# Performance work log

Hardware: AMD Instinct MI355X
Metric: run time of the kernel (lower is better)

Reference implementation:

```python
import jax, jax.numpy as jnp
import numpy as np

N_NODES = 50000
N_EDGES = 1_600_000
D_IN = 128
D_OUT = 128


def setup_inputs() -> dict:
    key = jax.random.key(0)
    k1, k2, k3, k4 = jax.random.split(key, 4)
    x = jax.random.normal(k1, (N_NODES, D_IN), dtype=jnp.float32)
    weight = jax.random.normal(k2, (D_IN, D_OUT), dtype=jnp.float32)
    bias = jnp.zeros((D_OUT,), dtype=jnp.float32)
    edge_row = jax.random.randint(k3, (N_EDGES,), 0, N_NODES, dtype=jnp.int64 if jax.config.jax_enable_x64 else jnp.int32)
    edge_col = jax.random.randint(k4, (N_EDGES,), 0, N_NODES, dtype=jnp.int64 if jax.config.jax_enable_x64 else jnp.int32)
    return {"x": x, "weight": weight, "bias": bias, "edge_row": edge_row, "edge_col": edge_col}


def reference(x, weight, bias, edge_row, edge_col):
    # edges_sparse is a binary [N, N] COO adjacency; edge (row=i, col=j) has value 1.
    n = x.shape[0]
    ones = jnp.ones(edge_row.shape[0], dtype=x.dtype)
    # out_degree = A.sum(dim=1): row sums of the adjacency
    out_degree = jax.ops.segment_sum(ones, edge_row, num_segments=n)
    deg_inv_sqrt = out_degree ** -0.5  # D = diag(deg^-0.5)
    # (D A D) x  ==  scatter_i sum_j deg_i^-0.5 * deg_j^-0.5 * x_j over edges (i, j)
    w = deg_inv_sqrt[edge_row] * deg_inv_sqrt[edge_col]  # [E]
    msg = w[:, None] * x[edge_col]                        # [E, D_IN]
    agg = jax.ops.segment_sum(msg, edge_row, num_segments=n)  # [N, D_IN]
    # dense projection + bias
    return agg @ weight + bias
```

## Files before the change

kernel.cpp:

```cpp
#include <hip/hip_runtime.h>
#include <hip/hip_bf16.h>

#define NODES   50000
#define EDGES   1600000
#define DIM     128
#define NB      391
#define BSTRIDE 4608
#define TILE    4096
#define EPT     16
#define NTILES  391
#define ZROW    50000

typedef unsigned int   u32;
typedef unsigned short u16;
typedef __attribute__((ext_vector_type(4))) float f32x4;
typedef __attribute__((ext_vector_type(8))) short s16x8;

__device__ inline u16 f2bf(float f) {
  __hip_bfloat16 h = __float2bfloat16(f);
  return *reinterpret_cast<u16*>(&h);
}

__global__ __launch_bounds__(256) void k_prep(const float* __restrict__ W,
                                              u16* __restrict__ wts,
                                              int* __restrict__ gcursor) {
  __shared__ float T[32 * 132];
  int t = threadIdx.x;
  int gi = blockIdx.x * 256 + t;
  if (gi < NB) gcursor[gi] = 0;
  int c0 = blockIdx.x * 32;
#pragma unroll
  for (int i = 0; i < 16; ++i) {
    int idx = i * 256 + t;
    int k = idx >> 5;
    int cc = idx & 31;
    T[cc * 132 + k] = W[k * 128 + c0 + cc];
  }
  __syncthreads();
#pragma unroll
  for (int i = 0; i < 2; ++i) {
    int idx = i * 256 + t;
    int cc = idx >> 4;
    int kc = idx & 15;
    int c = c0 + cc;
    int kbase = kc * 8;
    u32 p[4];
#pragma unroll
    for (int u = 0; u < 4; ++u) {
      float a = T[cc * 132 + kbase + 2 * u];
      float b = T[cc * 132 + kbase + 2 * u + 1];
      p[u] = (u32)f2bf(a) | ((u32)f2bf(b) << 16);
    }
    int off = c * 256 + ((kbase * 2) ^ ((c & 15) << 4));
    *(uint4*)((char*)wts + off) = make_uint4(p[0], p[1], p[2], p[3]);
  }
}

__global__ __launch_bounds__(256) void k_binA(const int* __restrict__ erow,
                                              const int* __restrict__ ecol,
                                              int* __restrict__ gcursor,
                                              u32* __restrict__ binned) {
  __shared__ int hist[NB];
  __shared__ int lcur[NB];
  int t = threadIdx.x;
  for (int b = t; b < NB; b += 256) hist[b] = 0;
  __syncthreads();
  int base = blockIdx.x * TILE;
  u32 v[EPT];
#pragma unroll
  for (int k = 0; k < 4; ++k) {
    int e4 = base + k * 1024 + t * 4;
    if (e4 < EDGES) {
      int4 rr = *(const int4*)&erow[e4];
      int4 cc = *(const int4*)&ecol[e4];
      v[k * 4 + 0] = ((u32)rr.x << 16) | (u32)cc.x;
      v[k * 4 + 1] = ((u32)rr.y << 16) | (u32)cc.y;
      v[k * 4 + 2] = ((u32)rr.z << 16) | (u32)cc.z;
      v[k * 4 + 3] = ((u32)rr.w << 16) | (u32)cc.w;
      atomicAdd(&hist[(u32)rr.x >> 7], 1);
      atomicAdd(&hist[(u32)rr.y >> 7], 1);
      atomicAdd(&hist[(u32)rr.z >> 7], 1);
      atomicAdd(&hist[(u32)rr.w >> 7], 1);
    } else {
      v[k * 4 + 0] = 0xffffffffu;
      v[k * 4 + 1] = 0xffffffffu;
      v[k * 4 + 2] = 0xffffffffu;
      v[k * 4 + 3] = 0xffffffffu;
    }
  }
  __syncthreads();
  for (int b = t; b < NB; b += 256) {
    int h = hist[b];
    lcur[b] = h ? (b * BSTRIDE + atomicAdd(&gcursor[b], h)) : 0;
  }
  __syncthreads();
#pragma unroll
  for (int k = 0; k < EPT; ++k) {
    if (v[k] != 0xffffffffu) {
      int b = (int)(v[k] >> 23);
      int pos = atomicAdd(&lcur[b], 1);
      if (pos < (b + 1) * BSTRIDE) binned[pos] = v[k];
    }
  }
}

__global__ __launch_bounds__(512) void k_binB(const u32* __restrict__ binned,
                                              const int* __restrict__ gcur,
                                              int2* __restrict__ rp2,
                                              float* __restrict__ dis,
                                              u16* __restrict__ cols) {
  __shared__ int cnt[128];
  __shared__ int sc[128];
  __shared__ int lcur[128];
  __shared__ u16 stage[BSTRIDE];
  int b = blockIdx.x;
  int t = threadIdx.x;
  int n0 = b << 7;
  int s = b * BSTRIDE;
  int cntE = gcur[b];
  if (cntE > BSTRIDE) cntE = BSTRIDE;
  int e = s + cntE;
  if (t < 128) cnt[t] = 0;
  __syncthreads();
  u32 held[9];
#pragma unroll
  for (int k = 0; k < 9; ++k) {
    int j = s + t + k * 512;
    u32 v = (j < e) ? binned[j] : 0xffffffffu;
    held[k] = v;
    if (v != 0xffffffffu) atomicAdd(&cnt[(int)(v >> 16) - n0], 1);
  }
  __syncthreads();
  if (t < 128) sc[t] = cnt[t];
  __syncthreads();
  for (int off = 1; off < 128; off <<= 1) {
    int tmp = (t >= off && t < 128) ? sc[t - off] : 0;
    __syncthreads();
    if (t < 128) sc[t] += tmp;
    __syncthreads();
  }
  if (t < 128) {
    int n = n0 + t;
    if (n < NODES) {
      int lexcl = sc[t] - cnt[t];
      rp2[n] = make_int2(s + lexcl, s + lexcl + cnt[t]);
      lcur[t] = lexcl;
      dis[n] = rsqrtf((float)cnt[t]);
    }
  }
  __syncthreads();
#pragma unroll
  for (int k = 0; k < 9; ++k) {
    u32 v = held[k];
    if (v != 0xffffffffu) {
      int pos = atomicAdd(&lcur[(int)(v >> 16) - n0], 1);
      stage[pos] = (u16)(v & 0xffffu);
    }
  }
  __syncthreads();
  {
    u32* dst = (u32*)(cols + s);
    const u32* src = (const u32*)stage;
    int nw = (cntE + 1) >> 1;
    for (int i = t; i < nw; i += 512) dst[i] = src[i];
  }
}

__global__ __launch_bounds__(256) void k_gemm(const float* __restrict__ x,
                                              const u16* __restrict__ wts,
                                              const float* __restrict__ dis,
                                              u16* __restrict__ y2) {
  __shared__ u16 xs[64 * 128];
  __shared__ u16 ws[128 * 128];
  const int t = threadIdx.x;
  const int bb = blockIdx.x * 64;

  {
    const uint4* src = (const uint4*)wts;
    uint4* dst = (uint4*)ws;
#pragma unroll
    for (int i = 0; i < 8; ++i) dst[i * 256 + t] = src[i * 256 + t];
  }
  {
#pragma unroll
    for (int i = 0; i < 8; ++i) {
      int goff = i * 4096 + t * 16;
      int row = goff >> 9;
      int gr = bb + row;
      float4 v = make_float4(0.f, 0.f, 0.f, 0.f);
      if (gr < NODES) v = *(const float4*)((const char*)x + (size_t)gr * 512 + (goff & 511));
      u32 lo = (u32)f2bf(v.x) | ((u32)f2bf(v.y) << 16);
      u32 hi = (u32)f2bf(v.z) | ((u32)f2bf(v.w) << 16);
      int colb = (goff & 511) >> 1;
      int off = row * 256 + (colb ^ ((row & 15) << 4));
      *(uint2*)((char*)xs + off) = make_uint2(lo, hi);
    }
  }
  __syncthreads();

  const int w = t >> 6, l = t & 63, m = l & 15, g = l >> 4;
  f32x4 acc[8];
#pragma unroll
  for (int j = 0; j < 8; ++j) acc[j] = (f32x4)0.0f;

  const char* xb = (const char*)xs;
  const char* wb = (const char*)ws;
  const int arow = w * 16 + m;
#pragma unroll
  for (int s = 0; s < 4; ++s) {
    int kx = (g * 16 + s * 64) ^ (m << 4);
    s16x8 a = *(const s16x8*)(xb + arow * 256 + kx);
#pragma unroll
    for (int j = 0; j < 8; ++j) {
      s16x8 b = *(const s16x8*)(wb + (j * 16 + m) * 256 + kx);
      acc[j] = __builtin_amdgcn_mfma_f32_16x16x32_bf16(a, b, acc[j], 0, 0, 0);
    }
  }

  int rbase = bb + w * 16 + g * 4;
  float4 d4 = *(const float4*)&dis[rbase];
#pragma unroll
  for (int j = 0; j < 8; ++j) {
#pragma unroll
    for (int r = 0; r < 4; ++r) {
      int gr = rbase + r;
      float dv = (r == 0) ? d4.x : (r == 1) ? d4.y : (r == 2) ? d4.z : d4.w;
      float val = (gr < NODES) ? acc[j][r] * dv : 0.0f;
      y2[(size_t)gr * 128 + j * 16 + m] = f2bf(val);
    }
  }
}

__global__ __launch_bounds__(256) void k_agg(const u16* __restrict__ y2,
                                             const int2* __restrict__ rp2,
                                             const u16* __restrict__ cols,
                                             const float* __restrict__ dis,
                                             const float* __restrict__ bias,
                                             float* __restrict__ out) {
  int node = (blockIdx.x * 256 + threadIdx.x) >> 6;
  int l = threadIdx.x & 63;
  if (node >= NODES) return;
  int q = l >> 4;
  int m = l & 15;
  int2 rr = rp2[node];
  int s = rr.x;
  int e = rr.y;

  float a0 = 0.f, a1 = 0.f, a2 = 0.f, a3 = 0.f;
  float a4 = 0.f, a5 = 0.f, a6 = 0.f, a7 = 0.f;
  const uint4* yb = (const uint4*)y2;

  int c0 = (s + q      < e) ? (int)cols[s + q]      : ZROW;
  int c1 = (s + 4 + q  < e) ? (int)cols[s + 4 + q]  : ZROW;
  int c2 = (s + 8 + q  < e) ? (int)cols[s + 8 + q]  : ZROW;
  int c3 = (s + 12 + q < e) ? (int)cols[s + 12 + q] : ZROW;

  for (int jb = s; jb < e; jb += 16) {
    int nb = jb + 16;
    int d0 = (nb + q      < e) ? (int)cols[nb + q]      : ZROW;
    int d1 = (nb + 4 + q  < e) ? (int)cols[nb + 4 + q]  : ZROW;
    int d2 = (nb + 8 + q  < e) ? (int)cols[nb + 8 + q]  : ZROW;
    int d3 = (nb + 12 + q < e) ? (int)cols[nb + 12 + q] : ZROW;
    uint4 v0 = yb[c0 * 16 + m];
    uint4 v1 = yb[c1 * 16 + m];
    uint4 v2 = yb[c2 * 16 + m];
    uint4 v3 = yb[c3 * 16 + m];
#define ACC(v)                                   \
    a0 += __uint_as_float((v).x << 16);          \
    a1 += __uint_as_float((v).x & 0xffff0000u);  \
    a2 += __uint_as_float((v).y << 16);          \
    a3 += __uint_as_float((v).y & 0xffff0000u);  \
    a4 += __uint_as_float((v).z << 16);          \
    a5 += __uint_as_float((v).z & 0xffff0000u);  \
    a6 += __uint_as_float((v).w << 16);          \
    a7 += __uint_as_float((v).w & 0xffff0000u);
    ACC(v0) ACC(v1) ACC(v2) ACC(v3)
#undef ACC
    c0 = d0; c1 = d1; c2 = d2; c3 = d3;
  }

  a0 += __shfl_xor(a0, 16); a0 += __shfl_xor(a0, 32);
  a1 += __shfl_xor(a1, 16); a1 += __shfl_xor(a1, 32);
  a2 += __shfl_xor(a2, 16); a2 += __shfl_xor(a2, 32);
  a3 += __shfl_xor(a3, 16); a3 += __shfl_xor(a3, 32);
  a4 += __shfl_xor(a4, 16); a4 += __shfl_xor(a4, 32);
  a5 += __shfl_xor(a5, 16); a5 += __shfl_xor(a5, 32);
  a6 += __shfl_xor(a6, 16); a6 += __shfl_xor(a6, 32);
  a7 += __shfl_xor(a7, 16); a7 += __shfl_xor(a7, 32);

  float di = (e > s) ? dis[node] : 0.0f;
  if (q < 2) {
    float r0 = q ? a4 : a0;
    float r1 = q ? a5 : a1;
    float r2 = q ? a6 : a2;
    float r3 = q ? a7 : a3;
    float4 bb = *(const float4*)&bias[m * 8 + q * 4];
    f32x4 o;
    o[0] = bb.x + di * r0;
    o[1] = bb.y + di * r1;
    o[2] = bb.z + di * r2;
    o[3] = bb.w + di * r3;
    __builtin_nontemporal_store(o, (f32x4*)&out[(size_t)node * 128 + m * 8 + q * 4]);
  }
}

extern "C" void kernel_launch(void* const* d_in, const int* in_sizes, int n_in,
                              void* d_out, int out_size, void* d_ws, size_t ws_size,
                              hipStream_t stream) {
  const float* x    = (const float*)d_in[0];
  const float* W    = (const float*)d_in[1];
  const float* bias = (const float*)d_in[2];
  const int*   erow = (const int*)d_in[3];
  const int*   ecol = (const int*)d_in[4];
  float* out = (float*)d_out;

  char* ws = (char*)d_ws;
  int*   gcursor = (int*)(ws + 0);
  int2*  rp2     = (int2*)(ws + 4096);
  float* dis     = (float*)(ws + 409600);
  u16*   wts     = (u16*)(ws + 614400);
  u32*   binned  = (u32*)(ws + 655360);
  u16*   cols    = (u16*)(ws + 7864320);
  u16*   y2      = (u16*)(ws + 11468800);

  k_prep<<<4, 256, 0, stream>>>(W, wts, gcursor);
  k_binA<<<NTILES, 256, 0, stream>>>(erow, ecol, gcursor, binned);
  k_binB<<<NB, 512, 0, stream>>>(binned, gcursor, rp2, dis, cols);
  k_gemm<<<(NODES + 63) / 64, 256, 0, stream>>>(x, wts, dis, y2);
  k_agg<<<(NODES * 64 + 255) / 256, 256, 0, stream>>>(y2, rp2, cols, dis, bias, out);
}
```

Before: 93.74 us.

## Merge edge binning and GEMM into one launch, apply source degree in aggregation

The edge binning kernel and the dense bf16 projection GEMM now run as two block ranges of a single launch. The GEMM no longer depends on degrees, so it can overlap with binning instead of waiting for k_binB. To allow this, the source-side deg^-0.5 scaling moves from the GEMM epilogue into the aggregation loop. That loop now does an extra gather of dis[col] per edge and a multiply per element. The padding entries of dis (including the ZROW sentinel) are zeroed in k_prep so sentinel columns contribute nothing.

```diff
diff --git a/kernel.cpp b/kernel.cpp
--- a/kernel.cpp
+++ b/kernel.cpp
@@ -23,11 +23,13 @@
 
 __global__ __launch_bounds__(256) void k_prep(const float* __restrict__ W,
                                               u16* __restrict__ wts,
-                                              int* __restrict__ gcursor) {
+                                              int* __restrict__ gcursor,
+                                              float* __restrict__ dis) {
   __shared__ float T[32 * 132];
   int t = threadIdx.x;
   int gi = blockIdx.x * 256 + t;
   if (gi < NB) gcursor[gi] = 0;
+  if (blockIdx.x == 0 && t < 48) dis[NODES + t] = 0.0f;
   int c0 = blockIdx.x * 32;
 #pragma unroll
   for (int i = 0; i < 16; ++i) {
@@ -56,50 +58,112 @@
   }
 }
 
-__global__ __launch_bounds__(256) void k_binA(const int* __restrict__ erow,
-                                              const int* __restrict__ ecol,
-                                              int* __restrict__ gcursor,
-                                              u32* __restrict__ binned) {
-  __shared__ int hist[NB];
-  __shared__ int lcur[NB];
-  int t = threadIdx.x;
-  for (int b = t; b < NB; b += 256) hist[b] = 0;
-  __syncthreads();
-  int base = blockIdx.x * TILE;
-  u32 v[EPT];
-#pragma unroll
-  for (int k = 0; k < 4; ++k) {
-    int e4 = base + k * 1024 + t * 4;
-    if (e4 < EDGES) {
-      int4 rr = *(const int4*)&erow[e4];
-      int4 cc = *(const int4*)&ecol[e4];
-      v[k * 4 + 0] = ((u32)rr.x << 16) | (u32)cc.x;
-      v[k * 4 + 1] = ((u32)rr.y << 16) | (u32)cc.y;
-      v[k * 4 + 2] = ((u32)rr.z << 16) | (u32)cc.z;
-      v[k * 4 + 3] = ((u32)rr.w << 16) | (u32)cc.w;
-      atomicAdd(&hist[(u32)rr.x >> 7], 1);
-      atomicAdd(&hist[(u32)rr.y >> 7], 1);
-      atomicAdd(&hist[(u32)rr.z >> 7], 1);
-      atomicAdd(&hist[(u32)rr.w >> 7], 1);
-    } else {
-      v[k * 4 + 0] = 0xffffffffu;
-      v[k * 4 + 1] = 0xffffffffu;
-      v[k * 4 + 2] = 0xffffffffu;
-      v[k * 4 + 3] = 0xffffffffu;
-    }
-  }
-  __syncthreads();
-  for (int b = t; b < NB; b += 256) {
-    int h = hist[b];
-    lcur[b] = h ? (b * BSTRIDE + atomicAdd(&gcursor[b], h)) : 0;
-  }
-  __syncthreads();
-#pragma unroll
-  for (int k = 0; k < EPT; ++k) {
-    if (v[k] != 0xffffffffu) {
-      int b = (int)(v[k] >> 23);
-      int pos = atomicAdd(&lcur[b], 1);
-      if (pos < (b + 1) * BSTRIDE) binned[pos] = v[k];
+__global__ __launch_bounds__(256) void k_ag(const int* __restrict__ erow,
+                                            const int* __restrict__ ecol,
+                                            const float* __restrict__ x,
+                                            const u16* __restrict__ wts,
+                                            int* __restrict__ gcursor,
+                                            u32* __restrict__ binned,
+                                            u16* __restrict__ y2) {
+  __shared__ u16 ws_[128 * 128];
+  __shared__ u16 xs_[64 * 128];
+  const int t = threadIdx.x;
+
+  if (blockIdx.x < NTILES) {
+    int* hist = (int*)ws_;
+    int* lcur = hist + NB;
+    for (int b = t; b < NB; b += 256) hist[b] = 0;
+    __syncthreads();
+    int base = blockIdx.x * TILE;
+    u32 v[EPT];
+#pragma unroll
+    for (int k = 0; k < 4; ++k) {
+      int e4 = base + k * 1024 + t * 4;
+      if (e4 < EDGES) {
+        int4 rr = *(const int4*)&erow[e4];
+        int4 cc = *(const int4*)&ecol[e4];
+        v[k * 4 + 0] = ((u32)rr.x << 16) | (u32)cc.x;
+        v[k * 4 + 1] = ((u32)rr.y << 16) | (u32)cc.y;
+        v[k * 4 + 2] = ((u32)rr.z << 16) | (u32)cc.z;
+        v[k * 4 + 3] = ((u32)rr.w << 16) | (u32)cc.w;
+        atomicAdd(&hist[(u32)rr.x >> 7], 1);
+        atomicAdd(&hist[(u32)rr.y >> 7], 1);
+        atomicAdd(&hist[(u32)rr.z >> 7], 1);
+        atomicAdd(&hist[(u32)rr.w >> 7], 1);
+      } else {
+        v[k * 4 + 0] = 0xffffffffu;
+        v[k * 4 + 1] = 0xffffffffu;
+        v[k * 4 + 2] = 0xffffffffu;
+        v[k * 4 + 3] = 0xffffffffu;
+      }
+    }
+    __syncthreads();
+    for (int b = t; b < NB; b += 256) {
+      int h = hist[b];
+      lcur[b] = h ? (b * BSTRIDE + atomicAdd(&gcursor[b], h)) : 0;
+    }
+    __syncthreads();
+#pragma unroll
+    for (int k = 0; k < EPT; ++k) {
+      if (v[k] != 0xffffffffu) {
+        int b = (int)(v[k] >> 23);
+        int pos = atomicAdd(&lcur[b], 1);
+        if (pos < (b + 1) * BSTRIDE) binned[pos] = v[k];
+      }
+    }
+  } else {
+    const int bb = (blockIdx.x - NTILES) * 64;
+    {
+      const uint4* src = (const uint4*)wts;
+      uint4* dst = (uint4*)ws_;
+#pragma unroll
+      for (int i = 0; i < 8; ++i) dst[i * 256 + t] = src[i * 256 + t];
+    }
+    {
+#pragma unroll
+      for (int i = 0; i < 8; ++i) {
+        int goff = i * 4096 + t * 16;
+        int row = goff >> 9;
+        int gr = bb + row;
+        float4 v = make_float4(0.f, 0.f, 0.f, 0.f);
+        if (gr < NODES) v = *(const float4*)((const char*)x + (size_t)gr * 512 + (goff & 511));
+        u32 lo = (u32)f2bf(v.x) | ((u32)f2bf(v.y) << 16);
+        u32 hi = (u32)f2bf(v.z) | ((u32)f2bf(v.w) << 16);
+        int colb = (goff & 511) >> 1;
+        int off = row * 256 + (colb ^ ((row & 15) << 4));
+        *(uint2*)((char*)xs_ + off) = make_uint2(lo, hi);
+      }
+    }
+    __syncthreads();
+
+    const int w = t >> 6, l = t & 63, m = l & 15, g = l >> 4;
+    f32x4 acc[8];
+#pragma unroll
+    for (int j = 0; j < 8; ++j) acc[j] = (f32x4)0.0f;
+
+    const char* xb = (const char*)xs_;
+    const char* wb = (const char*)ws_;
+    const int arow = w * 16 + m;
+#pragma unroll
+    for (int s = 0; s < 4; ++s) {
+      int kx = (g * 16 + s * 64) ^ (m << 4);
+      s16x8 a = *(const s16x8*)(xb + arow * 256 + kx);
+#pragma unroll
+      for (int j = 0; j < 8; ++j) {
+        s16x8 b = *(const s16x8*)(wb + (j * 16 + m) * 256 + kx);
+        acc[j] = __builtin_amdgcn_mfma_f32_16x16x32_bf16(a, b, acc[j], 0, 0, 0);
+      }
+    }
+
+    int rbase = bb + w * 16 + g * 4;
+#pragma unroll
+    for (int j = 0; j < 8; ++j) {
+#pragma unroll
+      for (int r = 0; r < 4; ++r) {
+        int gr = rbase + r;
+        float val = (gr < NODES) ? acc[j][r] : 0.0f;
+        y2[(size_t)gr * 128 + j * 16 + m] = f2bf(val);
+      }
     }
   }
 }
@@ -166,71 +230,6 @@
   }
 }
 
-__global__ __launch_bounds__(256) void k_gemm(const float* __restrict__ x,
-                                              const u16* __restrict__ wts,
-                                              const float* __restrict__ dis,
-                                              u16* __restrict__ y2) {
-  __shared__ u16 xs[64 * 128];
-  __shared__ u16 ws[128 * 128];
-  const int t = threadIdx.x;
-  const int bb = blockIdx.x * 64;
-
-  {
-    const uint4* src = (const uint4*)wts;
-    uint4* dst = (uint4*)ws;
-#pragma unroll
-    for (int i = 0; i < 8; ++i) dst[i * 256 + t] = src[i * 256 + t];
-  }
-  {
-#pragma unroll
-    for (int i = 0; i < 8; ++i) {
-      int goff = i * 4096 + t * 16;
-      int row = goff >> 9;
-      int gr = bb + row;
-      float4 v = make_float4(0.f, 0.f, 0.f, 0.f);
-      if (gr < NODES) v = *(const float4*)((const char*)x + (size_t)gr * 512 + (goff & 511));
-      u32 lo = (u32)f2bf(v.x) | ((u32)f2bf(v.y) << 16);
-      u32 hi = (u32)f2bf(v.z) | ((u32)f2bf(v.w) << 16);
-      int colb = (goff & 511) >> 1;
-      int off = row * 256 + (colb ^ ((row & 15) << 4));
-      *(uint2*)((char*)xs + off) = make_uint2(lo, hi);
-    }
-  }
-  __syncthreads();
-
-  const int w = t >> 6, l = t & 63, m = l & 15, g = l >> 4;
-  f32x4 acc[8];
-#pragma unroll
-  for (int j = 0; j < 8; ++j) acc[j] = (f32x4)0.0f;
-
-  const char* xb = (const char*)xs;
-  const char* wb = (const char*)ws;
-  const int arow = w * 16 + m;
-#pragma unroll
-  for (int s = 0; s < 4; ++s) {
-    int kx = (g * 16 + s * 64) ^ (m << 4);
-    s16x8 a = *(const s16x8*)(xb + arow * 256 + kx);
-#pragma unroll
-    for (int j = 0; j < 8; ++j) {
-      s16x8 b = *(const s16x8*)(wb + (j * 16 + m) * 256 + kx);
-      acc[j] = __builtin_amdgcn_mfma_f32_16x16x32_bf16(a, b, acc[j], 0, 0, 0);
-    }
-  }
-
-  int rbase = bb + w * 16 + g * 4;
-  float4 d4 = *(const float4*)&dis[rbase];
-#pragma unroll
-  for (int j = 0; j < 8; ++j) {
-#pragma unroll
-    for (int r = 0; r < 4; ++r) {
-      int gr = rbase + r;
-      float dv = (r == 0) ? d4.x : (r == 1) ? d4.y : (r == 2) ? d4.z : d4.w;
-      float val = (gr < NODES) ? acc[j][r] * dv : 0.0f;
-      y2[(size_t)gr * 128 + j * 16 + m] = f2bf(val);
-    }
-  }
-}
-
 __global__ __launch_bounds__(256) void k_agg(const u16* __restrict__ y2,
                                              const int2* __restrict__ rp2,
                                              const u16* __restrict__ cols,
@@ -261,20 +260,24 @@
     int d1 = (nb + 4 + q  < e) ? (int)cols[nb + 4 + q]  : ZROW;
     int d2 = (nb + 8 + q  < e) ? (int)cols[nb + 8 + q]  : ZROW;
     int d3 = (nb + 12 + q < e) ? (int)cols[nb + 12 + q] : ZROW;
+    float w0 = dis[c0];
+    float w1 = dis[c1];
+    float w2 = dis[c2];
+    float w3 = dis[c3];
     uint4 v0 = yb[c0 * 16 + m];
     uint4 v1 = yb[c1 * 16 + m];
     uint4 v2 = yb[c2 * 16 + m];
     uint4 v3 = yb[c3 * 16 + m];
-#define ACC(v)                                   \
-    a0 += __uint_as_float((v).x << 16);          \
-    a1 += __uint_as_float((v).x & 0xffff0000u);  \
-    a2 += __uint_as_float((v).y << 16);          \
-    a3 += __uint_as_float((v).y & 0xffff0000u);  \
-    a4 += __uint_as_float((v).z << 16);          \
-    a5 += __uint_as_float((v).z & 0xffff0000u);  \
-    a6 += __uint_as_float((v).w << 16);          \
-    a7 += __uint_as_float((v).w & 0xffff0000u);
-    ACC(v0) ACC(v1) ACC(v2) ACC(v3)
+#define ACC(v, wt)                                      \
+    a0 += (wt) * __uint_as_float((v).x << 16);          \
+    a1 += (wt) * __uint_as_float((v).x & 0xffff0000u);  \
+    a2 += (wt) * __uint_as_float((v).y << 16);          \
+    a3 += (wt) * __uint_as_float((v).y & 0xffff0000u);  \
+    a4 += (wt) * __uint_as_float((v).z << 16);          \
+    a5 += (wt) * __uint_as_float((v).z & 0xffff0000u);  \
+    a6 += (wt) * __uint_as_float((v).w << 16);          \
+    a7 += (wt) * __uint_as_float((v).w & 0xffff0000u);
+    ACC(v0, w0) ACC(v1, w1) ACC(v2, w2) ACC(v3, w3)
 #undef ACC
     c0 = d0; c1 = d1; c2 = d2; c3 = d3;
   }
@@ -323,9 +326,8 @@
   u16*   cols    = (u16*)(ws + 7864320);
   u16*   y2      = (u16*)(ws + 11468800);
 
-  k_prep<<<4, 256, 0, stream>>>(W, wts, gcursor);
-  k_binA<<<NTILES, 256, 0, stream>>>(erow, ecol, gcursor, binned);
+  k_prep<<<4, 256, 0, stream>>>(W, wts, gcursor, dis);
+  k_ag<<<NTILES + (NODES + 63) / 64, 256, 0, stream>>>(erow, ecol, x, wts, gcursor, binned, y2);
   k_binB<<<NB, 512, 0, stream>>>(binned, gcursor, rp2, dis, cols);
-  k_gemm<<<(NODES + 63) / 64, 256, 0, stream>>>(x, wts, dis, y2);
   k_agg<<<(NODES * 64 + 255) / 256, 256, 0, stream>>>(y2, rp2, cols, dis, bias, out);
 }
```

New measurement: 88.58 us. 1.06x faster.
